# Performance work log

Hardware: AMD Instinct MI355X
Metric: run time of the kernel (lower is better)

Reference implementation:

```python
import jax, jax.numpy as jnp
import numpy as np

N_NODES = 100000
N_EDGES = 640000
H_FEATS = 128


def setup_inputs() -> dict:
    key = jax.random.key(0)
    k_h, k_src, k_dst, k_w1, k_b1, k_w2, k_b2 = jax.random.split(key, 7)
    h = jax.random.normal(k_h, (N_NODES, H_FEATS), dtype=jnp.float32)
    src = jax.random.randint(k_src, (N_EDGES,), 0, N_NODES, dtype=jnp.int64)
    dst = jax.random.randint(k_dst, (N_EDGES,), 0, N_NODES, dtype=jnp.int64)
    # nn.Linear params: W1 (h_feats, 2*h_feats) as (out, in); store transposed for x @ W
    lim1 = 1.0 / np.sqrt(2 * H_FEATS)
    W1 = jax.random.uniform(k_w1, (2 * H_FEATS, H_FEATS), jnp.float32, -lim1, lim1)
    b1 = jax.random.uniform(k_b1, (H_FEATS,), jnp.float32, -lim1, lim1)
    lim2 = 1.0 / np.sqrt(H_FEATS)
    W2 = jax.random.uniform(k_w2, (H_FEATS, 1), jnp.float32, -lim2, lim2)
    b2 = jax.random.uniform(k_b2, (1,), jnp.float32, -lim2, lim2)
    return {"h": h, "src": src, "dst": dst, "W1": W1, "b1": b1, "W2": W2, "b2": b2}


def reference(h, src, dst, W1, b1, W2, b2):
    # gather src/dst node features per edge and concat: [E, 2*h_feats]
    he = jnp.concatenate([h[src], h[dst]], axis=1)
    hidden = jax.nn.relu(he @ W1 + b1)          # [E, h_feats]
    score = (hidden @ W2 + b2)[:, 0]            # [E]
    return score
```

## Files before the change

kernel.cpp:

```cpp
#include <hip/hip_runtime.h>

#define N_NODES 100000
#define N_EDGES 640000
#define F 128
#define NT 6250
#define NBLK 512

typedef __attribute__((ext_vector_type(8))) short short8;
typedef __attribute__((ext_vector_type(4))) float float4v;

static __device__ __forceinline__ unsigned short f2bf(float f) {
    unsigned int u = __float_as_uint(f);
    u += 0x7fffu + ((u >> 16) & 1u);
    return (unsigned short)(u >> 16);
}

__global__ __launch_bounds__(256) void prep_wt(
    const float* __restrict__ W1, unsigned short* __restrict__ Wt)
{
    int id = blockIdx.x * 256 + threadIdx.x;
    int n = id >> 7, k = id & 127;
    float v = W1[((n & 128) + k) * 128 + (n & 127)];
    Wt[id] = f2bf(v);
}

__global__ __launch_bounds__(256, 2) void node_proj(
    const float* __restrict__ h, const unsigned short* __restrict__ Wt,
    const float* __restrict__ b1,
    unsigned short* __restrict__ A, unsigned short* __restrict__ B)
{
    __shared__ unsigned short w_swz[256 * 128];
    __shared__ unsigned short hb[16 * 136];
    __shared__ unsigned short oA[16 * 136];
    __shared__ unsigned short oB[16 * 136];

    const int tid  = threadIdx.x;
    const int lane = tid & 63;
    const int l16  = lane & 15;
    const int quad = lane >> 4;
    const int w    = tid >> 6;

#pragma unroll
    for (int i = 0; i < 16; ++i) {
        int cl = i * 256 + tid;
        int r = cl >> 4, c = cl & 15;
        uint4 v = *(const uint4*)(Wt + (size_t)r * F + c * 8);
        *(uint4*)&w_swz[((r << 4) + (c ^ (r & 15))) * 8] = v;
    }

    const bool isA = (w < 2);
    const int colb = (w & 1) * 64;
    float4 bv[4];
#pragma unroll
    for (int p = 0; p < 4; ++p) {
        int col = colb + p * 16 + quad * 4;
        bv[p] = isA ? *(const float4*)(b1 + col) : make_float4(0.f, 0.f, 0.f, 0.f);
    }
    unsigned short* ostage = isA ? oA : oB;

    int srow[2], sc4[2];
#pragma unroll
    for (int i = 0; i < 2; ++i) { int f = i * 256 + tid; srow[i] = f >> 5; sc4[i] = f & 31; }

#define LOADH(PF, T)                                                           \
    _Pragma("unroll") for (int i = 0; i < 2; ++i)                              \
        PF[i] = *(const float4*)(h + ((size_t)(T) * 16 + srow[i]) * F + sc4[i] * 4);

#define CVTWRITE(PF)                                                           \
    _Pragma("unroll") for (int i = 0; i < 2; ++i) {                            \
        uint2 p;                                                               \
        p.x = (unsigned)f2bf(PF[i].x) | ((unsigned)f2bf(PF[i].y) << 16);       \
        p.y = (unsigned)f2bf(PF[i].z) | ((unsigned)f2bf(PF[i].w) << 16);       \
        *(uint2*)&hb[srow[i] * 136 + sc4[i] * 4] = p;                          \
    }

    int t = blockIdx.x;
    float4 pf[2];
    LOADH(pf, t); CVTWRITE(pf);
    __syncthreads();

    while (t < NT) {
        const int tn = t + NBLK;
        const bool actn = (tn < NT);
        if (actn) LOADH(pf, tn);

        float4v acc[4];
#pragma unroll
        for (int p = 0; p < 4; ++p) acc[p] = (float4v){0.f, 0.f, 0.f, 0.f};
#pragma unroll
        for (int k0 = 0; k0 < 4; ++k0) {
            short8 bf = *(const short8*)&hb[l16 * 136 + k0 * 32 + quad * 8];
            const int cc = (k0 * 4 + quad);
#pragma unroll
            for (int p = 0; p < 4; ++p) {
                const int row = w * 64 + p * 16 + l16;
                short8 af = *(const short8*)&w_swz[((row << 4) + (cc ^ l16)) * 8];
                acc[p] = __builtin_amdgcn_mfma_f32_16x16x32_bf16(af, bf, acc[p], 0, 0, 0);
            }
        }
        __syncthreads();

        if (actn) CVTWRITE(pf);
#pragma unroll
        for (int p = 0; p < 4; ++p) {
            ushort4 sv;
            sv.x = f2bf(acc[p][0] + bv[p].x);
            sv.y = f2bf(acc[p][1] + bv[p].y);
            sv.z = f2bf(acc[p][2] + bv[p].z);
            sv.w = f2bf(acc[p][3] + bv[p].w);
            *(ushort4*)&ostage[l16 * 136 + colb + p * 16 + quad * 4] = sv;
        }
        __syncthreads();

        {
            const int r = tid >> 4, c = tid & 15;
            const size_t goff = ((size_t)t * 16 + r) * F + c * 8;
            *(uint4*)(A + goff) = *(const uint4*)&oA[r * 136 + c * 8];
            *(uint4*)(B + goff) = *(const uint4*)&oB[r * 136 + c * 8];
        }
        t = tn;
    }
#undef LOADH
#undef CVTWRITE
}

__global__ __launch_bounds__(256) void edge_score(
    const unsigned short* __restrict__ A, const unsigned short* __restrict__ B,
    const int* __restrict__ src, const int* __restrict__ dst,
    const float* __restrict__ W2, const float* __restrict__ b2,
    float* __restrict__ out)
{
    const int tid = threadIdx.x;
    const int sub = tid & 7;
    const int e0  = blockIdx.x * 128 + (tid >> 3) * 4;

    const int4 sv = *(const int4*)(src + e0);
    const int4 dv = *(const int4*)(dst + e0);
    const int s[4] = {sv.x, sv.y, sv.z, sv.w};
    const int d[4] = {dv.x, dv.y, dv.z, dv.w};

    uint4 av0[4], av1[4], bv0[4], bv1[4];
#pragma unroll
    for (int i = 0; i < 4; ++i) {
        const unsigned short* Ar = A + (size_t)s[i] * F;
        const unsigned short* Br = B + (size_t)d[i] * F;
        av0[i] = *(const uint4*)(Ar + sub * 8);
        av1[i] = *(const uint4*)(Ar + 64 + sub * 8);
        bv0[i] = *(const uint4*)(Br + sub * 8);
        bv1[i] = *(const uint4*)(Br + 64 + sub * 8);
    }

    const float4 w0 = *(const float4*)(W2 + sub * 8);
    const float4 w1 = *(const float4*)(W2 + sub * 8 + 4);
    const float4 w2 = *(const float4*)(W2 + 64 + sub * 8);
    const float4 w3 = *(const float4*)(W2 + 64 + sub * 8 + 4);
    const float bias = b2[0];

#define TERM(UA, UB, WL, WH)                                                   \
    {                                                                          \
        float fa0 = __uint_as_float((UA) << 16);                               \
        float fa1 = __uint_as_float((UA) & 0xFFFF0000u);                       \
        float fb0 = __uint_as_float((UB) << 16);                               \
        float fb1 = __uint_as_float((UB) & 0xFFFF0000u);                       \
        sacc = fmaf(fmaxf(fa0 + fb0, 0.f), (WL), sacc);                        \
        sacc = fmaf(fmaxf(fa1 + fb1, 0.f), (WH), sacc);                        \
    }
#pragma unroll
    for (int i = 0; i < 4; ++i) {
        float sacc = 0.f;
        TERM(av0[i].x, bv0[i].x, w0.x, w0.y)
        TERM(av0[i].y, bv0[i].y, w0.z, w0.w)
        TERM(av0[i].z, bv0[i].z, w1.x, w1.y)
        TERM(av0[i].w, bv0[i].w, w1.z, w1.w)
        TERM(av1[i].x, bv1[i].x, w2.x, w2.y)
        TERM(av1[i].y, bv1[i].y, w2.z, w2.w)
        TERM(av1[i].z, bv1[i].z, w3.x, w3.y)
        TERM(av1[i].w, bv1[i].w, w3.z, w3.w)
        sacc += __shfl_xor(sacc, 1);
        sacc += __shfl_xor(sacc, 2);
        sacc += __shfl_xor(sacc, 4);
        if (sub == 0) out[e0 + i] = sacc + bias;
    }
#undef TERM
}

extern "C" void kernel_launch(void* const* d_in, const int* in_sizes, int n_in,
                              void* d_out, int out_size, void* d_ws, size_t ws_size,
                              hipStream_t stream) {
    const float* h   = (const float*)d_in[0];
    const int*   src = (const int*)d_in[1];
    const int*   dst = (const int*)d_in[2];
    const float* W1  = (const float*)d_in[3];
    const float* b1  = (const float*)d_in[4];
    const float* W2  = (const float*)d_in[5];
    const float* b2  = (const float*)d_in[6];
    float* out = (float*)d_out;

    unsigned short* Wt = (unsigned short*)d_ws;
    unsigned short* A  = Wt + 256 * 128;
    unsigned short* B  = A + (size_t)N_NODES * F;

    prep_wt<<<128, 256, 0, stream>>>(W1, Wt);
    node_proj<<<NBLK, 256, 0, stream>>>(h, Wt, b1, A, B);
    edge_score<<<N_EDGES / 128, 256, 0, stream>>>(A, B, src, dst, W2, b2, out);
}
```

Before: 155.0 us.

## Restructure node projection: 512-thread blocks, 32-row tiles, double-buffered staging

The node projection kernel now runs 256 blocks of 512 threads, each processing 32-node tiles with a 2x2 MFMA register tile per wave. The input and output LDS staging is double-buffered, which removes one __syncthreads per iteration and lets the global store of the previous tile overlap with the current tile's compute. Each block loads the full weight matrix into LDS once, so there are half as many blocks repeating that load. In exchange, per-CU occupancy drops to one large block and LDS use rises.

Result: no change. 156.4 us (+1.0%).

```diff
diff --git a/kernel.cpp b/kernel.cpp
--- a/kernel.cpp
+++ b/kernel.cpp
@@ -3,8 +3,8 @@
 #define N_NODES 100000
 #define N_EDGES 640000
 #define F 128
-#define NT 6250
-#define NBLK 512
+#define NT32 3125
+#define NPB 256
 
 typedef __attribute__((ext_vector_type(8))) short short8;
 typedef __attribute__((ext_vector_type(4))) float float4v;
@@ -24,15 +24,15 @@
     Wt[id] = f2bf(v);
 }
 
-__global__ __launch_bounds__(256, 2) void node_proj(
+__global__ __launch_bounds__(512, 1) void node_proj(
     const float* __restrict__ h, const unsigned short* __restrict__ Wt,
     const float* __restrict__ b1,
     unsigned short* __restrict__ A, unsigned short* __restrict__ B)
 {
     __shared__ unsigned short w_swz[256 * 128];
-    __shared__ unsigned short hb[16 * 136];
-    __shared__ unsigned short oA[16 * 136];
-    __shared__ unsigned short oB[16 * 136];
+    __shared__ unsigned short hb[2][32 * 136];
+    __shared__ unsigned short oA[2][32 * 132];
+    __shared__ unsigned short oB[2][32 * 132];
 
     const int tid  = threadIdx.x;
     const int lane = tid & 63;
@@ -41,84 +41,104 @@
     const int w    = tid >> 6;
 
 #pragma unroll
-    for (int i = 0; i < 16; ++i) {
-        int cl = i * 256 + tid;
+    for (int i = 0; i < 8; ++i) {
+        int cl = i * 512 + tid;
         int r = cl >> 4, c = cl & 15;
         uint4 v = *(const uint4*)(Wt + (size_t)r * F + c * 8);
         *(uint4*)&w_swz[((r << 4) + (c ^ (r & 15))) * 8] = v;
     }
 
-    const bool isA = (w < 2);
-    const int colb = (w & 1) * 64;
-    float4 bv[4];
-#pragma unroll
-    for (int p = 0; p < 4; ++p) {
+    const bool isA = (w < 4);
+    const int colb = (w & 3) * 32;
+    float4 bv[2];
+#pragma unroll
+    for (int p = 0; p < 2; ++p) {
         int col = colb + p * 16 + quad * 4;
         bv[p] = isA ? *(const float4*)(b1 + col) : make_float4(0.f, 0.f, 0.f, 0.f);
     }
-    unsigned short* ostage = isA ? oA : oB;
 
     int srow[2], sc4[2];
 #pragma unroll
-    for (int i = 0; i < 2; ++i) { int f = i * 256 + tid; srow[i] = f >> 5; sc4[i] = f & 31; }
+    for (int i = 0; i < 2; ++i) { int f = i * 512 + tid; srow[i] = f >> 5; sc4[i] = f & 31; }
 
 #define LOADH(PF, T)                                                           \
     _Pragma("unroll") for (int i = 0; i < 2; ++i)                              \
-        PF[i] = *(const float4*)(h + ((size_t)(T) * 16 + srow[i]) * F + sc4[i] * 4);
-
-#define CVTWRITE(PF)                                                           \
+        PF[i] = *(const float4*)(h + ((size_t)(T) * 32 + srow[i]) * F + sc4[i] * 4);
+
+#define CVTWRITE(PF, DST)                                                      \
     _Pragma("unroll") for (int i = 0; i < 2; ++i) {                            \
         uint2 p;                                                               \
         p.x = (unsigned)f2bf(PF[i].x) | ((unsigned)f2bf(PF[i].y) << 16);       \
         p.y = (unsigned)f2bf(PF[i].z) | ((unsigned)f2bf(PF[i].w) << 16);       \
-        *(uint2*)&hb[srow[i] * 136 + sc4[i] * 4] = p;                          \
-    }
+        *(uint2*)&(DST)[srow[i] * 136 + sc4[i] * 4] = p;                       \
+    }
+
+    const int strow = tid >> 4, stc = tid & 15;
 
     int t = blockIdx.x;
     float4 pf[2];
-    LOADH(pf, t); CVTWRITE(pf);
+    LOADH(pf, t); CVTWRITE(pf, hb[0]);
     __syncthreads();
 
-    while (t < NT) {
-        const int tn = t + NBLK;
-        const bool actn = (tn < NT);
+    int cur = 0, pb = 0, tprev = -1;
+    while (t < NT32) {
+        const int tn = t + NPB;
+        const bool actn = (tn < NT32);
         if (actn) LOADH(pf, tn);
 
-        float4v acc[4];
-#pragma unroll
-        for (int p = 0; p < 4; ++p) acc[p] = (float4v){0.f, 0.f, 0.f, 0.f};
+        if (tprev >= 0) {
+            const size_t goff = ((size_t)tprev * 32 + strow) * F + stc * 8;
+            *(uint4*)(A + goff) = *(const uint4*)&oA[pb ^ 1][strow * 132 + stc * 8];
+            *(uint4*)(B + goff) = *(const uint4*)&oB[pb ^ 1][strow * 132 + stc * 8];
+        }
+
+        float4v acc[2][2];
+#pragma unroll
+        for (int p = 0; p < 2; ++p)
+#pragma unroll
+            for (int nt = 0; nt < 2; ++nt) acc[p][nt] = (float4v){0.f, 0.f, 0.f, 0.f};
 #pragma unroll
         for (int k0 = 0; k0 < 4; ++k0) {
-            short8 bf = *(const short8*)&hb[l16 * 136 + k0 * 32 + quad * 8];
-            const int cc = (k0 * 4 + quad);
-#pragma unroll
-            for (int p = 0; p < 4; ++p) {
-                const int row = w * 64 + p * 16 + l16;
+            const int kb = k0 * 32 + quad * 8;
+            short8 bf[2];
+#pragma unroll
+            for (int nt = 0; nt < 2; ++nt)
+                bf[nt] = *(const short8*)&hb[cur][(nt * 16 + l16) * 136 + kb];
+            const int cc = k0 * 4 + quad;
+#pragma unroll
+            for (int p = 0; p < 2; ++p) {
+                const int row = w * 32 + p * 16 + l16;
                 short8 af = *(const short8*)&w_swz[((row << 4) + (cc ^ l16)) * 8];
-                acc[p] = __builtin_amdgcn_mfma_f32_16x16x32_bf16(af, bf, acc[p], 0, 0, 0);
+#pragma unroll
+                for (int nt = 0; nt < 2; ++nt)
+                    acc[p][nt] = __builtin_amdgcn_mfma_f32_16x16x32_bf16(
+                        af, bf[nt], acc[p][nt], 0, 0, 0);
             }
         }
-        __syncthreads();
-
-        if (actn) CVTWRITE(pf);
-#pragma unroll
-        for (int p = 0; p < 4; ++p) {
-            ushort4 sv;
-            sv.x = f2bf(acc[p][0] + bv[p].x);
-            sv.y = f2bf(acc[p][1] + bv[p].y);
-            sv.z = f2bf(acc[p][2] + bv[p].z);
-            sv.w = f2bf(acc[p][3] + bv[p].w);
-            *(ushort4*)&ostage[l16 * 136 + colb + p * 16 + quad * 4] = sv;
+
+        if (actn) CVTWRITE(pf, hb[cur ^ 1]);
+
+        {
+            unsigned short* ost = (isA ? oA : oB)[pb];
+#pragma unroll
+            for (int p = 0; p < 2; ++p)
+#pragma unroll
+                for (int nt = 0; nt < 2; ++nt) {
+                    ushort4 sv;
+                    sv.x = f2bf(acc[p][nt][0] + bv[p].x);
+                    sv.y = f2bf(acc[p][nt][1] + bv[p].y);
+                    sv.z = f2bf(acc[p][nt][2] + bv[p].z);
+                    sv.w = f2bf(acc[p][nt][3] + bv[p].w);
+                    *(ushort4*)&ost[(nt * 16 + l16) * 132 + colb + p * 16 + quad * 4] = sv;
+                }
         }
         __syncthreads();
-
-        {
-            const int r = tid >> 4, c = tid & 15;
-            const size_t goff = ((size_t)t * 16 + r) * F + c * 8;
-            *(uint4*)(A + goff) = *(const uint4*)&oA[r * 136 + c * 8];
-            *(uint4*)(B + goff) = *(const uint4*)&oB[r * 136 + c * 8];
-        }
-        t = tn;
+        tprev = t; t = tn; cur ^= 1; pb ^= 1;
+    }
+    if (tprev >= 0) {
+        const size_t goff = ((size_t)tprev * 32 + strow) * F + stc * 8;
+        *(uint4*)(A + goff) = *(const uint4*)&oA[pb ^ 1][strow * 132 + stc * 8];
+        *(uint4*)(B + goff) = *(const uint4*)&oB[pb ^ 1][strow * 132 + stc * 8];
     }
 #undef LOADH
 #undef CVTWRITE
@@ -201,6 +221,6 @@
     unsigned short* B  = A + (size_t)N_NODES * F;
 
     prep_wt<<<128, 256, 0, stream>>>(W1, Wt);
-    node_proj<<<NBLK, 256, 0, stream>>>(h, Wt, b1, A, B);
+    node_proj<<<NPB, 512, 0, stream>>>(h, Wt, b1, A, B);
     edge_score<<<N_EDGES / 128, 256, 0, stream>>>(A, B, src, dst, W2, b2, out);
 }
```

## Split node projection across blockIdx.y halves and double-buffer LDS stages

Applied to the files above, without the earlier changes.

The node projection kernel now splits the A and B weight halves across a second grid dimension, so each block holds only 128 rows of W in LDS, and it launches 768x2 blocks at occupancy 3. The h tile and output staging buffers are double-buffered, which removes one barrier per iteration. The global store of the previous tile is deferred so it overlaps with the next tile's MFMAs. The trade-off is that each block now reads h, so h is loaded twice overall.

Result: no change. 157.2 us (+1.4%).

```diff
diff --git a/kernel.cpp b/kernel.cpp
--- a/kernel.cpp
+++ b/kernel.cpp
@@ -4,7 +4,7 @@
 #define N_EDGES 640000
 #define F 128
 #define NT 6250
-#define NBLK 512
+#define NPB 768
 
 typedef __attribute__((ext_vector_type(8))) short short8;
 typedef __attribute__((ext_vector_type(4))) float float4v;
@@ -24,39 +24,39 @@
     Wt[id] = f2bf(v);
 }
 
-__global__ __launch_bounds__(256, 2) void node_proj(
+__global__ __launch_bounds__(256, 3) void node_proj(
     const float* __restrict__ h, const unsigned short* __restrict__ Wt,
     const float* __restrict__ b1,
     unsigned short* __restrict__ A, unsigned short* __restrict__ B)
 {
-    __shared__ unsigned short w_swz[256 * 128];
-    __shared__ unsigned short hb[16 * 136];
-    __shared__ unsigned short oA[16 * 136];
-    __shared__ unsigned short oB[16 * 136];
+    __shared__ unsigned short w_swz[128 * 128];
+    __shared__ unsigned short hb[2][16 * 136];
+    __shared__ unsigned short ox[2][16 * 132];
 
     const int tid  = threadIdx.x;
     const int lane = tid & 63;
     const int l16  = lane & 15;
     const int quad = lane >> 4;
     const int w    = tid >> 6;
-
-#pragma unroll
-    for (int i = 0; i < 16; ++i) {
+    const int y    = blockIdx.y;
+
+#pragma unroll
+    for (int i = 0; i < 8; ++i) {
         int cl = i * 256 + tid;
         int r = cl >> 4, c = cl & 15;
-        uint4 v = *(const uint4*)(Wt + (size_t)r * F + c * 8);
+        uint4 v = *(const uint4*)(Wt + (size_t)(y * 128 + r) * F + c * 8);
         *(uint4*)&w_swz[((r << 4) + (c ^ (r & 15))) * 8] = v;
     }
 
-    const bool isA = (w < 2);
-    const int colb = (w & 1) * 64;
-    float4 bv[4];
-#pragma unroll
-    for (int p = 0; p < 4; ++p) {
+    const bool isA = (y == 0);
+    const int colb = w * 32;
+    float4 bv[2];
+#pragma unroll
+    for (int p = 0; p < 2; ++p) {
         int col = colb + p * 16 + quad * 4;
         bv[p] = isA ? *(const float4*)(b1 + col) : make_float4(0.f, 0.f, 0.f, 0.f);
     }
-    unsigned short* ostage = isA ? oA : oB;
+    unsigned short* outp = isA ? A : B;
 
     int srow[2], sc4[2];
 #pragma unroll
@@ -66,59 +66,64 @@
     _Pragma("unroll") for (int i = 0; i < 2; ++i)                              \
         PF[i] = *(const float4*)(h + ((size_t)(T) * 16 + srow[i]) * F + sc4[i] * 4);
 
-#define CVTWRITE(PF)                                                           \
+#define CVTWRITE(PF, DST)                                                      \
     _Pragma("unroll") for (int i = 0; i < 2; ++i) {                            \
         uint2 p;                                                               \
         p.x = (unsigned)f2bf(PF[i].x) | ((unsigned)f2bf(PF[i].y) << 16);       \
         p.y = (unsigned)f2bf(PF[i].z) | ((unsigned)f2bf(PF[i].w) << 16);       \
-        *(uint2*)&hb[srow[i] * 136 + sc4[i] * 4] = p;                          \
-    }
+        *(uint2*)&(DST)[srow[i] * 136 + sc4[i] * 4] = p;                       \
+    }
+
+    const int strow = tid >> 4, stc = tid & 15;
 
     int t = blockIdx.x;
     float4 pf[2];
-    LOADH(pf, t); CVTWRITE(pf);
+    LOADH(pf, t); CVTWRITE(pf, hb[0]);
     __syncthreads();
 
+    int cur = 0, pb = 0, tprev = -1;
     while (t < NT) {
-        const int tn = t + NBLK;
+        const int tn = t + NPB;
         const bool actn = (tn < NT);
         if (actn) LOADH(pf, tn);
 
-        float4v acc[4];
-#pragma unroll
-        for (int p = 0; p < 4; ++p) acc[p] = (float4v){0.f, 0.f, 0.f, 0.f};
+        if (tprev >= 0) {
+            const size_t goff = ((size_t)tprev * 16 + strow) * F + stc * 8;
+            *(uint4*)(outp + goff) = *(const uint4*)&ox[pb ^ 1][strow * 132 + stc * 8];
+        }
+
+        float4v acc[2];
+#pragma unroll
+        for (int p = 0; p < 2; ++p) acc[p] = (float4v){0.f, 0.f, 0.f, 0.f};
 #pragma unroll
         for (int k0 = 0; k0 < 4; ++k0) {
-            short8 bf = *(const short8*)&hb[l16 * 136 + k0 * 32 + quad * 8];
-            const int cc = (k0 * 4 + quad);
-#pragma unroll
-            for (int p = 0; p < 4; ++p) {
-                const int row = w * 64 + p * 16 + l16;
+            short8 bf = *(const short8*)&hb[cur][l16 * 136 + k0 * 32 + quad * 8];
+            const int cc = k0 * 4 + quad;
+#pragma unroll
+            for (int p = 0; p < 2; ++p) {
+                const int row = colb + p * 16 + l16;
                 short8 af = *(const short8*)&w_swz[((row << 4) + (cc ^ l16)) * 8];
                 acc[p] = __builtin_amdgcn_mfma_f32_16x16x32_bf16(af, bf, acc[p], 0, 0, 0);
             }
         }
-        __syncthreads();
-
-        if (actn) CVTWRITE(pf);
-#pragma unroll
-        for (int p = 0; p < 4; ++p) {
+
+        if (actn) CVTWRITE(pf, hb[cur ^ 1]);
+
+#pragma unroll
+        for (int p = 0; p < 2; ++p) {
             ushort4 sv;
             sv.x = f2bf(acc[p][0] + bv[p].x);
             sv.y = f2bf(acc[p][1] + bv[p].y);
             sv.z = f2bf(acc[p][2] + bv[p].z);
             sv.w = f2bf(acc[p][3] + bv[p].w);
-            *(ushort4*)&ostage[l16 * 136 + colb + p * 16 + quad * 4] = sv;
+            *(ushort4*)&ox[pb][l16 * 132 + colb + p * 16 + quad * 4] = sv;
         }
         __syncthreads();
-
-        {
-            const int r = tid >> 4, c = tid & 15;
-            const size_t goff = ((size_t)t * 16 + r) * F + c * 8;
-            *(uint4*)(A + goff) = *(const uint4*)&oA[r * 136 + c * 8];
-            *(uint4*)(B + goff) = *(const uint4*)&oB[r * 136 + c * 8];
-        }
-        t = tn;
+        tprev = t; t = tn; cur ^= 1; pb ^= 1;
+    }
+    if (tprev >= 0) {
+        const size_t goff = ((size_t)tprev * 16 + strow) * F + stc * 8;
+        *(uint4*)(outp + goff) = *(const uint4*)&ox[pb ^ 1][strow * 132 + stc * 8];
     }
 #undef LOADH
 #undef CVTWRITE
@@ -201,6 +206,6 @@
     unsigned short* B  = A + (size_t)N_NODES * F;
 
     prep_wt<<<128, 256, 0, stream>>>(W1, Wt);
-    node_proj<<<NBLK, 256, 0, stream>>>(h, Wt, b1, A, B);
+    node_proj<<<dim3(NPB, 2), 256, 0, stream>>>(h, Wt, b1, A, B);
     edge_score<<<N_EDGES / 128, 256, 0, stream>>>(A, B, src, dst, W2, b2, out);
 }
```
